# Optimization experiments

Measured on AMD Instinct MI355X. Metric: run time of the kernel, lower is better.

## Reference

```python
import jax, jax.numpy as jnp
import numpy as np

N = 100_000      # nodes
E = 3_200_000    # edges (avg degree 32)
F_IN = 128       # in_channels
HID = 64         # hidden_channels
G = 64           # graphs in batch


def setup_inputs() -> dict:
    key = jax.random.key(0)
    k0, k1, k2, k3 = jax.random.split(key, 4)
    x = jax.random.normal(k0, (N, F_IN), jnp.float32)
    edge_index = jax.random.randint(k1, (2, E), 0, N, dtype=jnp.int32)
    # sorted graph assignment, every graph non-empty
    batch = (jnp.arange(N, dtype=jnp.int32) * G) // N
    W1 = jax.random.normal(k2, (F_IN, HID), jnp.float32) * (1.0 / np.sqrt(F_IN))
    b1 = jnp.zeros((HID,), jnp.float32)
    W2 = jax.random.normal(k3, (HID, 1), jnp.float32) * (1.0 / np.sqrt(HID))
    b2 = jnp.zeros((1,), jnp.float32)
    return {"x": x, "edge_index": edge_index, "batch": batch,
            "W1": W1, "b1": b1, "W2": W2, "b2": b2}


def gcn_layer(x, src, dst, W, b):
    """GCNConv: add self-loops, symmetric deg^-1/2 norm, scatter-add, bias."""
    h = x @ W  # transform first (smaller messages)
    loops = jnp.arange(N, dtype=src.dtype)
    s = jnp.concatenate([src, loops])
    d = jnp.concatenate([dst, loops])
    deg = jax.ops.segment_sum(jnp.ones(s.shape[0], x.dtype), d, num_segments=N)
    dinv = jnp.where(deg > 0, jax.lax.rsqrt(deg), 0.0)
    norm = dinv[s] * dinv[d]                         # [E+N]
    out = jax.ops.segment_sum(h[s] * norm[:, None], d, num_segments=N)
    return out + b


def reference(x, edge_index, batch, W1, b1, W2, b2):
    src, dst = edge_index[0], edge_index[1]
    h = jax.nn.relu(gcn_layer(x, src, dst, W1, b1))
    h = gcn_layer(h, src, dst, W2, b2)               # [N, 1]
    counts = jax.ops.segment_sum(jnp.ones(N, jnp.int32), batch, num_segments=G)
    big_node_idx = jnp.cumsum(counts) - 1            # last node of each graph
    return h[big_node_idx].squeeze(-1)               # [G]
```

## Files before the change

kernel.cpp:

```cpp
#include <hip/hip_runtime.h>

#define N_NODES 100000
#define N_EDGES 3200000
#define F_IN    128
#define HID     64
#define NGRAPH  64

#define NBUK    196
#define BSHIFT  9
#define BCAP    18432
#define CHUNK   5120
#define NBLK_A  625
#define SLICES  16
#define NWORDS  3200
#define MAXDEG  96
#define NIDCAP  4096
#define L2CAP   8192


__device__ __forceinline__ bool is_big(int v, const int* __restrict__ batch) {
    return (v == N_NODES - 1) || (batch[v] != batch[v + 1]);
}
__device__ __forceinline__ float dinv_of(int degv) {
    return rsqrtf((float)(degv + 1));
}

__global__ void k_init(const int* __restrict__ batch, unsigned* __restrict__ bigmask,
                       unsigned* __restrict__ nmask, int* __restrict__ nid_of,
                       int* __restrict__ nlist, int* __restrict__ counters,
                       float* __restrict__ out) {
    if (blockIdx.x == 0 && threadIdx.x < NGRAPH) out[threadIdx.x] = 0.f;
    int v = blockIdx.x * 256 + threadIdx.x;
    if (v >= N_NODES) return;
    if (is_big(v, batch)) {
        atomicOr(&bigmask[v >> 5], 1u << (v & 31));
        atomicOr(&nmask[v >> 5], 1u << (v & 31));
        int p = atomicAdd(&counters[2], 1);
        nid_of[v] = p;
        nlist[p]  = v;
    }
}

__global__ __launch_bounds__(256) void k_partA(const int* __restrict__ src,
        const int* __restrict__ dst, const unsigned* __restrict__ bigmask,
        unsigned* __restrict__ nmask, unsigned* __restrict__ plist,
        int* __restrict__ bcnt, int2* __restrict__ l2list, int* __restrict__ counters) {
    __shared__ unsigned staged[CHUNK];
    __shared__ unsigned char sbkt[CHUNK];
    __shared__ int hist4[4][NBUK];
    __shared__ int startb[256];
    __shared__ int curb[NBUK], gbasea[NBUK];
    __shared__ int2 l2buf[64];
    __shared__ int l2n, l2base;
    const int t = threadIdx.x;
    for (int i = t; i < NBUK; i += 256) {
        hist4[0][i] = 0; hist4[1][i] = 0; hist4[2][i] = 0; hist4[3][i] = 0;
    }
    if (t == 0) l2n = 0;
    __syncthreads();

    const int w = t >> 6;
    const int E0 = blockIdx.x * CHUNK;
    const int4* s4 = (const int4*)(src + E0);
    const int4* d4 = (const int4*)(dst + E0);
    int vloc[20]; unsigned pk[20];
#pragma unroll
    for (int it = 0; it < 5; ++it) {
        int4 dd = d4[t + it * 256];
        int4 ss = s4[t + it * 256];
        int vv[4] = {dd.x, dd.y, dd.z, dd.w};
        int uu[4] = {ss.x, ss.y, ss.z, ss.w};
#pragma unroll
        for (int j = 0; j < 4; ++j) {
            int v = vv[j], u = uu[j];
            vloc[it * 4 + j] = v;
            pk[it * 4 + j] = ((unsigned)u << BSHIFT) | (unsigned)(v & 511);
            atomicAdd(&hist4[w][v >> BSHIFT], 1);
            if ((bigmask[v >> 5] >> (v & 31)) & 1) {
                atomicOr(&nmask[u >> 5], 1u << (u & 31));
                int p = atomicAdd(&l2n, 1);
                if (p < 64) l2buf[p] = make_int2(u, v);
            }
        }
    }
    __syncthreads();
    int c = 0;
    if (t < NBUK) c = hist4[0][t] + hist4[1][t] + hist4[2][t] + hist4[3][t];
    startb[t] = c;
    __syncthreads();
    for (int off = 1; off < 256; off <<= 1) {
        int val = (t >= off) ? startb[t - off] : 0;
        __syncthreads();
        startb[t] += val;
        __syncthreads();
    }
    startb[t] -= c;
    if (t < NBUK) {
        curb[t]   = startb[t];
        gbasea[t] = atomicAdd(&bcnt[t], c);
    }
    if (t == 0 && l2n > 0) {
        int ln = l2n; if (ln > 64) ln = 64;
        l2base = atomicAdd(&counters[1], ln);
    }
    __syncthreads();
    {
        int ln = l2n; if (ln > 64) ln = 64;
        for (int i = t; i < ln; i += 256) {
            int p = l2base + i;
            if (p < L2CAP) l2list[p] = l2buf[i];
        }
    }
#pragma unroll
    for (int it = 0; it < 20; ++it) {
        int b = vloc[it] >> BSHIFT;
        int pos = atomicAdd(&curb[b], 1);
        staged[pos] = pk[it];
        sbkt[pos]   = (unsigned char)b;
    }
    __syncthreads();
    for (int i = t; i < CHUNK; i += 256) {
        int b = sbkt[i];
        int s = gbasea[b] + (i - startb[b]);
        if (s < BCAP) plist[(size_t)b * BCAP + s] = staged[i];
    }
}

__global__ void k_buildnid(const unsigned* __restrict__ nmask,
                           const unsigned* __restrict__ bigmask,
                           int* __restrict__ nid_of, int* __restrict__ nlist,
                           int* __restrict__ counters) {
    int w = blockIdx.x * 256 + threadIdx.x;
    unsigned m = (w < NWORDS) ? (nmask[w] & ~bigmask[w]) : 0u;
    int c = __popc(m);
    __shared__ int sc[256];
    __shared__ int gbase;
    sc[threadIdx.x] = c;
    __syncthreads();
    for (int off = 1; off < 256; off <<= 1) {
        int t = (threadIdx.x >= off) ? sc[threadIdx.x - off] : 0;
        __syncthreads();
        sc[threadIdx.x] += t;
        __syncthreads();
    }
    if (threadIdx.x == 0) gbase = atomicAdd(&counters[2], sc[255]);
    __syncthreads();
    int p = gbase + sc[threadIdx.x] - c;
    while (m) {
        int b = __ffs(m) - 1; m &= m - 1;
        int v = w * 32 + b;
        if (p < NIDCAP) { nid_of[v] = p; nlist[p] = v; }
        p++;
    }
}

__global__ __launch_bounds__(256) void k_partB(const unsigned* __restrict__ plist,
        const int* __restrict__ bcnt, const unsigned* __restrict__ nmask,
        const int* __restrict__ nid_of, int* __restrict__ incnt,
        int* __restrict__ csr, int* __restrict__ deg) {
    __shared__ int bins[512];
    __shared__ unsigned nm16[16];
    const int b = blockIdx.x / SLICES, s = blockIdx.x % SLICES;
    for (int i = threadIdx.x; i < 512; i += 256) bins[i] = 0;
    if (threadIdx.x < 16) nm16[threadIdx.x] = nmask[b * 16 + threadIdx.x];
    __syncthreads();
    int n = bcnt[b]; if (n > BCAP) n = BCAP;
    const int i0 = (int)((long)n * s / SLICES);
    const int i1 = (int)((long)n * (s + 1) / SLICES);
    const unsigned* lp = plist + (size_t)b * BCAP;
    const int lo = b << BSHIFT;
    for (int i = i0 + threadIdx.x; i < i1; i += 256) {
        unsigned e = lp[i];
        int local = (int)(e & 511u);
        atomicAdd(&bins[local], 1);
        if ((nm16[local >> 5] >> (local & 31)) & 1) {
            int nid = nid_of[lo + local];
            int slot = atomicAdd(&incnt[nid], 1);
            if (slot < MAXDEG) csr[nid * MAXDEG + slot] = (int)(e >> BSHIFT);
        }
    }
    __syncthreads();
    for (int i = threadIdx.x; i < 512; i += 256) {
        int v = lo + i, c = bins[i];
        if (c > 0 && v < N_NODES) atomicAdd(&deg[v], c);
    }
}

__global__ __launch_bounds__(256) void k_xaggtrans(const int* __restrict__ nlist,
        const int* __restrict__ incnt, const int* __restrict__ csr,
        const int* __restrict__ deg, const float* __restrict__ x,
        const float* __restrict__ W1, const float* __restrict__ b1,
        const float* __restrict__ W2, const int* __restrict__ counters,
        float* __restrict__ h2s) {
    __shared__ float4 sm[8][32];
    __shared__ float xaggL[F_IN];
    __shared__ float p2[4 * HID];
    int ncnt = counters[2]; if (ncnt > NIDCAP) ncnt = NIDCAP;
    const int tid = threadIdx.x;
    const int l = tid & 31, g = tid >> 5;
    const int f = tid & 63, gg = tid >> 6;
    for (int nid = blockIdx.x; nid < ncnt; nid += gridDim.x) {
        int v = nlist[nid];
        int m = incnt[nid]; if (m > MAXDEG) m = MAXDEG;
        const int* cs = csr + nid * MAXDEG;
        float4 acc = make_float4(0.f, 0.f, 0.f, 0.f);
        for (int j = g; j < m; j += 8) {
            int u = cs[j];
            float du = dinv_of(deg[u]);
            float4 xr = ((const float4*)(x + (size_t)u * F_IN))[l];
            acc.x += du * xr.x; acc.y += du * xr.y;
            acc.z += du * xr.z; acc.w += du * xr.w;
        }
        sm[g][l] = acc;
        __syncthreads();
        if (tid < 32) {
            float4 tot = make_float4(0.f, 0.f, 0.f, 0.f);
#pragma unroll
            for (int k = 0; k < 8; ++k) {
                float4 p = sm[k][tid];
                tot.x += p.x; tot.y += p.y; tot.z += p.z; tot.w += p.w;
            }
            float dv = dinv_of(deg[v]);
            float4 xv = ((const float4*)(x + (size_t)v * F_IN))[tid];
            float4 r;
            r.x = dv * tot.x + dv * dv * xv.x;
            r.y = dv * tot.y + dv * dv * xv.y;
            r.z = dv * tot.z + dv * dv * xv.z;
            r.w = dv * tot.w + dv * dv * xv.w;
            ((float4*)xaggL)[tid] = r;
        }
        __syncthreads();
        float a = 0.f;
#pragma unroll
        for (int k0 = 0; k0 < 32; ++k0) {
            int k = gg * 32 + k0;
            a += xaggL[k] * W1[(size_t)k * HID + f];
        }
        p2[gg * HID + f] = a;
        __syncthreads();
        if (tid < HID) {
            float h = p2[tid] + p2[HID + tid] + p2[2 * HID + tid] + p2[3 * HID + tid] + b1[tid];
            float cc = fmaxf(h, 0.f) * W2[tid];
#pragma unroll
            for (int off = 32; off > 0; off >>= 1) cc += __shfl_down(cc, off, 64);
            if (tid == 0) h2s[nid] = cc;
        }
        __syncthreads();
    }
}

__global__ void k_agg2(const int2* __restrict__ l2list, const int* __restrict__ counters,
                       const int* __restrict__ deg, const float* __restrict__ h2s,
                       const int* __restrict__ batch, const int* __restrict__ nlist,
                       const int* __restrict__ nid_of, const float* __restrict__ b2,
                       float* __restrict__ out) {
    if (blockIdx.x == 0 && threadIdx.x < NGRAPH) {
        int v = nlist[threadIdx.x];
        float di = dinv_of(deg[v]);
        atomicAdd(&out[batch[v]], di * di * h2s[threadIdx.x] + b2[0]);
    }
    int tid = blockIdx.x * 256 + threadIdx.x;
    int nt  = gridDim.x * 256;
    int n   = counters[1];
    if (n > L2CAP) n = L2CAP;
    for (int i = tid; i < n; i += nt) {
        int2 e = l2list[i];
        float dx = dinv_of(deg[e.x]);
        float dy = dinv_of(deg[e.y]);
        atomicAdd(&out[batch[e.y]], dx * dy * h2s[nid_of[e.x]]);
    }
}

extern "C" void kernel_launch(void* const* d_in, const int* in_sizes, int n_in,
                              void* d_out, int out_size, void* d_ws, size_t ws_size,
                              hipStream_t stream) {
    const float* x     = (const float*)d_in[0];
    const int*   eidx  = (const int*)d_in[1];
    const int*   src   = eidx;
    const int*   dst   = eidx + N_EDGES;
    const int*   batch = (const int*)d_in[2];
    const float* W1    = (const float*)d_in[3];
    const float* b1    = (const float*)d_in[4];
    const float* W2    = (const float*)d_in[5];
    const float* b2    = (const float*)d_in[6];
    float*       out   = (float*)d_out;

    char* ws = (char*)d_ws;
    size_t off = 0;
    int*      counters = (int*)(ws + off);      off += 256;
    int*      bcnt     = (int*)(ws + off);      off += 1024;
    unsigned* nmask    = (unsigned*)(ws + off); off += NWORDS * 4;
    unsigned* bigmask  = (unsigned*)(ws + off); off += NWORDS * 4;
    int*      incnt    = (int*)(ws + off);      off += NIDCAP * 4;
    int*      deg      = (int*)(ws + off);      off += (size_t)N_NODES * 4;
    size_t zero_bytes = off;
    int*      nid_of   = (int*)(ws + off);      off += (size_t)N_NODES * 4;
    int*      nlist    = (int*)(ws + off);      off += (size_t)NIDCAP * 4;
    float*    h2s      = (float*)(ws + off);    off += (size_t)NIDCAP * 4;
    int2*     l2list   = (int2*)(ws + off);     off += (size_t)L2CAP * 8;
    int*      csr      = (int*)(ws + off);      off += (size_t)NIDCAP * MAXDEG * 4;
    unsigned* plist    = (unsigned*)(ws + off); off += (size_t)NBUK * BCAP * 4;
    if (off > ws_size) return;

    hipMemsetAsync(d_ws, 0, zero_bytes, stream);

    const int BN = (N_NODES + 255) / 256;

    k_init<<<BN, 256, 0, stream>>>(batch, bigmask, nmask, nid_of, nlist, counters, out);
    k_partA<<<NBLK_A, 256, 0, stream>>>(src, dst, bigmask, nmask, plist, bcnt, l2list, counters);
    k_buildnid<<<(NWORDS + 255) / 256, 256, 0, stream>>>(nmask, bigmask, nid_of, nlist, counters);
    k_partB<<<NBUK * SLICES, 256, 0, stream>>>(plist, bcnt, nmask, nid_of, incnt, csr, deg);
    k_xaggtrans<<<2048, 256, 0, stream>>>(nlist, incnt, csr, deg, x, W1, b1, W2, counters, h2s);
    k_agg2<<<8, 256, 0, stream>>>(l2list, counters, deg, h2s, batch, nlist, nid_of, b2, out);
}
```

Measured before the change: 174.7 us.

## Fuse final aggregation into transform kernel via last-block tail, warp-scan histogram

```diff
diff --git a/kernel.cpp b/kernel.cpp
--- a/kernel.cpp
+++ b/kernel.cpp
@@ -11,11 +11,12 @@
 #define BCAP    18432
 #define CHUNK   5120
 #define NBLK_A  625
-#define SLICES  16
+#define SLICES  8
 #define NWORDS  3200
 #define MAXDEG  96
 #define NIDCAP  4096
 #define L2CAP   8192
+#define NBLK_X  2048
 
 
 __device__ __forceinline__ bool is_big(int v, const int* __restrict__ batch) {
@@ -50,16 +51,18 @@
     __shared__ int hist4[4][NBUK];
     __shared__ int startb[256];
     __shared__ int curb[NBUK], gbasea[NBUK];
+    __shared__ int wsum[4];
     __shared__ int2 l2buf[64];
     __shared__ int l2n, l2base;
     const int t = threadIdx.x;
+    const int lane = t & 63;
+    const int w = t >> 6;
     for (int i = t; i < NBUK; i += 256) {
         hist4[0][i] = 0; hist4[1][i] = 0; hist4[2][i] = 0; hist4[3][i] = 0;
     }
     if (t == 0) l2n = 0;
     __syncthreads();
 
-    const int w = t >> 6;
     const int E0 = blockIdx.x * CHUNK;
     const int4* s4 = (const int4*)(src + E0);
     const int4* d4 = (const int4*)(dst + E0);
@@ -86,17 +89,21 @@
     __syncthreads();
     int c = 0;
     if (t < NBUK) c = hist4[0][t] + hist4[1][t] + hist4[2][t] + hist4[3][t];
-    startb[t] = c;
-    __syncthreads();
-    for (int off = 1; off < 256; off <<= 1) {
-        int val = (t >= off) ? startb[t - off] : 0;
-        __syncthreads();
-        startb[t] += val;
-        __syncthreads();
-    }
-    startb[t] -= c;
+    int sc = c;
+#pragma unroll
+    for (int off = 1; off < 64; off <<= 1) {
+        int y = __shfl_up(sc, off, 64);
+        if (lane >= off) sc += y;
+    }
+    if (lane == 63) wsum[w] = sc;
+    __syncthreads();
+    int pre = 0;
+#pragma unroll
+    for (int k = 0; k < 4; ++k) pre += (k < w) ? wsum[k] : 0;
+    int excl = pre + sc - c;
+    startb[t] = excl;
     if (t < NBUK) {
-        curb[t]   = startb[t];
+        curb[t]   = excl;
         gbasea[t] = atomicAdd(&bcnt[t], c);
     }
     if (t == 0 && l2n > 0) {
@@ -159,10 +166,8 @@
         const int* __restrict__ nid_of, int* __restrict__ incnt,
         int* __restrict__ csr, int* __restrict__ deg) {
     __shared__ int bins[512];
-    __shared__ unsigned nm16[16];
     const int b = blockIdx.x / SLICES, s = blockIdx.x % SLICES;
     for (int i = threadIdx.x; i < 512; i += 256) bins[i] = 0;
-    if (threadIdx.x < 16) nm16[threadIdx.x] = nmask[b * 16 + threadIdx.x];
     __syncthreads();
     int n = bcnt[b]; if (n > BCAP) n = BCAP;
     const int i0 = (int)((long)n * s / SLICES);
@@ -173,8 +178,9 @@
         unsigned e = lp[i];
         int local = (int)(e & 511u);
         atomicAdd(&bins[local], 1);
-        if ((nm16[local >> 5] >> (local & 31)) & 1) {
-            int nid = nid_of[lo + local];
+        int v = lo + local;
+        if ((nmask[v >> 5] >> (v & 31)) & 1) {
+            int nid = nid_of[v];
             int slot = atomicAdd(&incnt[nid], 1);
             if (slot < MAXDEG) csr[nid * MAXDEG + slot] = (int)(e >> BSHIFT);
         }
@@ -191,10 +197,14 @@
         const int* __restrict__ deg, const float* __restrict__ x,
         const float* __restrict__ W1, const float* __restrict__ b1,
         const float* __restrict__ W2, const int* __restrict__ counters,
-        float* __restrict__ h2s) {
+        float* __restrict__ h2s, int* __restrict__ donecnt,
+        const int2* __restrict__ l2list, const int* __restrict__ batch,
+        const int* __restrict__ nid_of, const float* __restrict__ b2,
+        float* __restrict__ out) {
     __shared__ float4 sm[8][32];
     __shared__ float xaggL[F_IN];
     __shared__ float p2[4 * HID];
+    __shared__ int lastf;
     int ncnt = counters[2]; if (ncnt > NIDCAP) ncnt = NIDCAP;
     const int tid = threadIdx.x;
     const int l = tid & 31, g = tid >> 5;
@@ -247,23 +257,18 @@
         }
         __syncthreads();
     }
-}
-
-__global__ void k_agg2(const int2* __restrict__ l2list, const int* __restrict__ counters,
-                       const int* __restrict__ deg, const float* __restrict__ h2s,
-                       const int* __restrict__ batch, const int* __restrict__ nlist,
-                       const int* __restrict__ nid_of, const float* __restrict__ b2,
-                       float* __restrict__ out) {
-    if (blockIdx.x == 0 && threadIdx.x < NGRAPH) {
-        int v = nlist[threadIdx.x];
+    __threadfence();
+    if (tid == 0) lastf = (atomicAdd(donecnt, 1) == (int)gridDim.x - 1);
+    __syncthreads();
+    if (!lastf) return;
+    __threadfence();
+    if (tid < NGRAPH) {
+        int v = nlist[tid];
         float di = dinv_of(deg[v]);
-        atomicAdd(&out[batch[v]], di * di * h2s[threadIdx.x] + b2[0]);
-    }
-    int tid = blockIdx.x * 256 + threadIdx.x;
-    int nt  = gridDim.x * 256;
-    int n   = counters[1];
-    if (n > L2CAP) n = L2CAP;
-    for (int i = tid; i < n; i += nt) {
+        atomicAdd(&out[batch[v]], di * di * h2s[tid] + b2[0]);
+    }
+    int n = counters[1]; if (n > L2CAP) n = L2CAP;
+    for (int i = tid; i < n; i += 256) {
         int2 e = l2list[i];
         float dx = dinv_of(deg[e.x]);
         float dy = dinv_of(deg[e.y]);
@@ -288,6 +293,7 @@
     char* ws = (char*)d_ws;
     size_t off = 0;
     int*      counters = (int*)(ws + off);      off += 256;
+    int*      donecnt  = (int*)(ws + off);      off += 256;
     int*      bcnt     = (int*)(ws + off);      off += 1024;
     unsigned* nmask    = (unsigned*)(ws + off); off += NWORDS * 4;
     unsigned* bigmask  = (unsigned*)(ws + off); off += NWORDS * 4;
@@ -310,6 +316,6 @@
     k_partA<<<NBLK_A, 256, 0, stream>>>(src, dst, bigmask, nmask, plist, bcnt, l2list, counters);
     k_buildnid<<<(NWORDS + 255) / 256, 256, 0, stream>>>(nmask, bigmask, nid_of, nlist, counters);
     k_partB<<<NBUK * SLICES, 256, 0, stream>>>(plist, bcnt, nmask, nid_of, incnt, csr, deg);
-    k_xaggtrans<<<2048, 256, 0, stream>>>(nlist, incnt, csr, deg, x, W1, b1, W2, counters, h2s);
-    k_agg2<<<8, 256, 0, stream>>>(l2list, counters, deg, h2s, batch, nlist, nid_of, b2, out);
-}
+    k_xaggtrans<<<NBLK_X, 256, 0, stream>>>(nlist, incnt, csr, deg, x, W1, b1, W2, counters,
+                                            h2s, donecnt, l2list, batch, nid_of, b2, out);
+}
```

Result: slower. 316.9 us (+81.4%).
